# Kernel tuning notes

Hardware: AMD Instinct MI355X
Metric: run time of the kernel (lower is better)

The kernel has to match this reference:

```python
import jax, jax.numpy as jnp
import numpy as np

B, IN, OUT, E, K = 8192, 512, 720, 16, 2
MOE_TEMP = 1.0


def setup_inputs() -> dict:
    key = jax.random.key(0)
    ks = jax.random.split(key, 5)
    s_in = 1.0 / np.sqrt(IN)
    return {
        "x": jax.random.normal(ks[0], (B, IN), dtype=jnp.float32),
        "Wg": jax.random.normal(ks[1], (IN, E), dtype=jnp.float32) * s_in,
        "bg": jax.random.normal(ks[2], (E,), dtype=jnp.float32) * 0.01,
        "We": jax.random.normal(ks[3], (E, IN, OUT), dtype=jnp.float32) * s_in,
        "be": jax.random.normal(ks[4], (E, OUT), dtype=jnp.float32) * 0.01,
    }


def reference(x, Wg, bg, We, be):
    # Gating (eval mode: no noise, divide by temperature)
    gate = (x @ Wg + bg) / MOE_TEMP                      # [B, E]
    topk_vals, topk_idx = jax.lax.top_k(gate, K)          # [B, K]
    gates = jax.nn.softmax(topk_vals, axis=1)             # [B, K]

    # Dense all-expert forward (as the original module computes)
    expert_out = jnp.einsum('bi,eio->beo', x, We) + be    # [B, E, OUT]
    sel = jnp.take_along_axis(expert_out, topk_idx[:, :, None], axis=1)  # [B, K, OUT]
    output = jnp.sum(gates[:, :, None] * sel, axis=1)     # [B, OUT]

    # Load-balancing loss
    probs = jax.nn.softmax(gate, axis=1)                  # [B, E]
    assign = jnp.argmax(gate, axis=1)                     # [B]
    D = jnp.zeros((E,), dtype=gate.dtype).at[assign].add(1.0) / x.shape[0]
    P = jnp.mean(probs, axis=0)
    lb_loss = jnp.sum(D * P) * E
    return output, lb_loss
```

## Files before the change

### kernel.cpp

```cpp
#include <hip/hip_runtime.h>
#include <hip/hip_bf16.h>


#define BATCH 8192
#define IND   512
#define OUTD  720
#define NEXP  16
#define CPAD  16
#define NGBLK 512

typedef __attribute__((ext_vector_type(8))) short short8;
typedef __attribute__((ext_vector_type(4))) float floatx4;

__device__ __forceinline__ unsigned short f2bf(float f) {
    union { float f; unsigned u; } v; v.f = f;
    unsigned r = v.u + 0x7FFFu + ((v.u >> 16) & 1u);
    return (unsigned short)(r >> 16);
}
__device__ __forceinline__ float bf2f(unsigned short u) {
    union { unsigned u; float f; } v; v.u = ((unsigned)u) << 16;
    return v.f;
}

__device__ __forceinline__ void gl2lds16(const void* g, void* l) {
    __builtin_amdgcn_global_load_lds(
        (const __attribute__((address_space(1))) void*)g,
        (__attribute__((address_space(3))) void*)l, 16, 0, 0);
}

__global__ __launch_bounds__(256) void prep_kernel(
    const float* __restrict__ x, const float* __restrict__ Wg,
    const float* __restrict__ bg, const float* __restrict__ We,
    float* __restrict__ gates, int* __restrict__ rowinfo,
    int* __restrict__ cnt_blk, float* __restrict__ Pblk, float* __restrict__ Dblk,
    unsigned short* __restrict__ xb, unsigned short* __restrict__ Wt)
{
    __shared__ __align__(16) char smem[35328];
    int tid = threadIdx.x;

    if (blockIdx.x < NGBLK) {
        float* sWg   = (float*)smem;
        float* sg    = sWg + 16 * 516;
        float* smax  = sg + 16 * 17;
        float* sinv  = smax + 16;
        int*   sasgn = (int*)(sinv + 16);

        int rbase = blockIdx.x * 16;

        const float4* gw4 = (const float4*)Wg;
        #pragma unroll
        for (int j = 0; j < 8; ++j) {
            int f = tid + j * 256;
            float4 v = gw4[f];
            int i  = f >> 2;
            int e0 = (f & 3) * 4;
            sWg[(e0 + 0) * 516 + i] = v.x;
            sWg[(e0 + 1) * 516 + i] = v.y;
            sWg[(e0 + 2) * 516 + i] = v.z;
            sWg[(e0 + 3) * 516 + i] = v.w;
        }

        const float4* gx4 = (const float4*)(x + (size_t)rbase * IND);
        #pragma unroll
        for (int j = 0; j < 4; ++j) {
            int f = tid + j * 256;
            float4 v0 = gx4[2 * f];
            float4 v1 = gx4[2 * f + 1];
            short8 o;
            o[0] = (short)f2bf(v0.x); o[1] = (short)f2bf(v0.y);
            o[2] = (short)f2bf(v0.z); o[3] = (short)f2bf(v0.w);
            o[4] = (short)f2bf(v1.x); o[5] = (short)f2bf(v1.y);
            o[6] = (short)f2bf(v1.z); o[7] = (short)f2bf(v1.w);
            *(short8*)&xb[(size_t)rbase * IND + (size_t)f * 8] = o;
        }
        __syncthreads();

        int r = tid >> 4, e = tid & 15;
        const float4* xr = (const float4*)(x + (size_t)(rbase + r) * IND);
        const float4* wr = (const float4*)&sWg[e * 516];
        float acc = bg[e];
        #pragma unroll 8
        for (int i4 = 0; i4 < 128; ++i4) {
            float4 a = xr[i4], w = wr[i4];
            acc += a.x * w.x + a.y * w.y + a.z * w.z + a.w * w.w;
        }
        sg[r * 17 + e] = acc;
        __syncthreads();

        if (tid < 16) {
            int row = rbase + tid;
            float v0 = -1e30f, v1 = -1e30f; int i0 = 0, i1 = 0;
            float g[16];
            #pragma unroll
            for (int ee = 0; ee < 16; ++ee) {
                float v = sg[tid * 17 + ee]; g[ee] = v;
                if (v > v0)      { v1 = v0; i1 = i0; v0 = v; i0 = ee; }
                else if (v > v1) { v1 = v;  i1 = ee; }
            }
            float e1   = expf(v1 - v0);
            float inv2 = 1.f / (1.f + e1);
            gates[row * 2 + 0] = inv2;
            gates[row * 2 + 1] = e1 * inv2;

            float s = 0.f;
            #pragma unroll
            for (int ee = 0; ee < 16; ++ee) s += expf(g[ee] - v0);
            smax[tid]  = v0;
            sinv[tid]  = 1.f / s;
            sasgn[tid] = i0 | (i1 << 8);
        }
        __syncthreads();

        if (tid < 16) {
            int me  = sasgn[tid];
            int i0  = me & 255, i1 = me >> 8;
            int p0 = 0, p1 = 0;
            for (int rp = 0; rp < tid; ++rp) {
                int a = sasgn[rp];
                int a0 = a & 255, a1 = a >> 8;
                p0 += (a0 == i0) + (a1 == i0);
                p1 += (a0 == i1) + (a1 == i1);
            }
            rowinfo[rbase + tid] = i0 | (i1 << 4) | (p0 << 8) | (p1 << 13);

            int ee = tid;
            int cnt = 0; float D = 0.f, P = 0.f;
            #pragma unroll
            for (int rp = 0; rp < 16; ++rp) {
                int a = sasgn[rp];
                int a0 = a & 255, a1 = a >> 8;
                cnt += (a0 == ee) + (a1 == ee);
                D   += (a0 == ee) ? 1.f : 0.f;
                P   += expf(sg[rp * 17 + ee] - smax[rp]) * sinv[rp];
            }
            cnt_blk[blockIdx.x * 16 + ee] = cnt;
            Dblk[blockIdx.x * 16 + ee]    = D;
            Pblk[blockIdx.x * 16 + ee]    = P;
        }
    } else {
        float* tile = (float*)smem;
        int t  = blockIdx.x - NGBLK;
        int e  = t / 184;
        int rem = t - e * 184;
        int kb = (rem / 23) * 64;
        int ob = (rem % 23) * 32;
        const float* src = We + (size_t)e * (IND * OUTD);

        #pragma unroll
        for (int p = 0; p < 2; ++p) {
            int f  = tid + p * 256;
            int kk = f >> 3;
            int o4 = f & 7;
            float4 v = make_float4(0.f, 0.f, 0.f, 0.f);
            if (ob + o4 * 4 < OUTD)
                v = *(const float4*)&src[(size_t)(kb + kk) * OUTD + ob + o4 * 4];
            tile[(o4 * 4 + 0) * 69 + kk] = v.x;
            tile[(o4 * 4 + 1) * 69 + kk] = v.y;
            tile[(o4 * 4 + 2) * 69 + kk] = v.z;
            tile[(o4 * 4 + 3) * 69 + kk] = v.w;
        }
        __syncthreads();

        int o  = tid >> 3;
        int k8 = tid & 7;
        if (ob + o < OUTD) {
            const float* sp = &tile[o * 69 + k8 * 8];
            short8 w;
            #pragma unroll
            for (int q = 0; q < 8; ++q) w[q] = (short)f2bf(sp[q]);
            *(short8*)&Wt[(size_t)e * (OUTD * IND) + (size_t)(ob + o) * IND + kb + k8 * 8] = w;
        }
    }
}

__global__ __launch_bounds__(256) void scan_kernel(
    const int* __restrict__ cnt_blk, const float* __restrict__ Pblk,
    const float* __restrict__ Dblk,
    int* __restrict__ base_blk, int* __restrict__ counts,
    float* __restrict__ Psum, float* __restrict__ Dsum)
{
    __shared__ int scnt[NGBLK * 16];
    __shared__ float sredP[256], sredD[256];
    int tid = threadIdx.x;

    #pragma unroll
    for (int j = 0; j < 32; ++j) scnt[tid + j * 256] = cnt_blk[tid + j * 256];
    __syncthreads();

    if (tid < 16) {
        int run = 0;
        for (int b = 0; b < NGBLK; ++b) {
            int c = scnt[b * 16 + tid];
            scnt[b * 16 + tid] = run;
            run += c;
        }
        counts[tid * CPAD] = run;
    }
    __syncthreads();

    #pragma unroll
    for (int j = 0; j < 32; ++j) base_blk[tid + j * 256] = scnt[tid + j * 256];

    int e = tid & 15, stripe = tid >> 4;
    float accP = 0.f, accD = 0.f;
    for (int j = 0; j < 32; ++j) {
        int b = stripe * 32 + j;
        accP += Pblk[b * 16 + e];
        accD += Dblk[b * 16 + e];
    }
    sredP[tid] = accP; sredD[tid] = accD;
    __syncthreads();
    if (tid < 16) {
        float P = 0.f, D = 0.f;
        #pragma unroll
        for (int s = 0; s < 16; ++s) { P += sredP[s * 16 + tid]; D += sredD[s * 16 + tid]; }
        Psum[tid * CPAD] = P;
        Dsum[tid * CPAD] = D;
    }
}

__global__ __launch_bounds__(256) void scatter_kernel(
    const int* __restrict__ rowinfo, const int* __restrict__ base_blk,
    unsigned short* __restrict__ lists, int* __restrict__ inv)
{
    int row = blockIdx.x * 256 + threadIdx.x;
    int info = rowinfo[row];
    int i0 = info & 15, i1 = (info >> 4) & 15;
    int p0 = (info >> 8) & 31, p1 = (info >> 13) & 31;
    int b = row >> 4;
    int pos0 = base_blk[b * 16 + i0] + p0;
    int pos1 = base_blk[b * 16 + i1] + p1;
    lists[i0 * BATCH + pos0] = (unsigned short)(row << 1);
    lists[i1 * BATCH + pos1] = (unsigned short)((row << 1) | 1);
    inv[row * 2 + 0] = i0 * BATCH + pos0;
    inv[row * 2 + 1] = i1 * BATCH + pos1;
}

__global__ __launch_bounds__(256, 4) void moe_mfma_kernel(
    const unsigned short* __restrict__ xb, const unsigned short* __restrict__ Wt,
    const float* __restrict__ be,
    const int* __restrict__ counts, const float* __restrict__ gates,
    const unsigned short* __restrict__ lists,
    unsigned short* __restrict__ partial, int use_inv)
{
    int e = blockIdx.z;
    int n = counts[e * CPAD];
    int r0 = blockIdx.y * 128;
    if (r0 >= n) return;
    int n0 = blockIdx.x * 96;

    __shared__ unsigned short sAB[14336];
    __shared__ int   srow[128];
    __shared__ float sgw[128];
    __shared__ unsigned short sent[128];

    int tid = threadIdx.x;
    if (tid < 128) {
        int idx = r0 + tid;
        if (idx < n) {
            int ent = lists[e * BATCH + idx];
            srow[tid] = ent >> 1;
            sgw[tid]  = gates[(ent >> 1) * 2 + (ent & 1)];
            sent[tid] = (unsigned short)ent;
        } else { srow[tid] = 0; sgw[tid] = 0.f; sent[tid] = 0; }
    }
    __syncthreads();

    int lane = tid & 63, wave = tid >> 6;
    int lsub = lane >> 3;
    int swz  = (lane & 7) ^ lsub;

    const unsigned short* aglb[4];
    unsigned short* alds[4];
    #pragma unroll
    for (int g = 0; g < 4; ++g) {
        int row = wave * 32 + g * 8 + lsub;
        aglb[g] = xb + (size_t)srow[row] * IND + swz * 8;
        alds[g] = &sAB[(wave * 32 + g * 8) * 64];
    }
    const unsigned short* bglb[3];
    unsigned short* blds[3];
    #pragma unroll
    for (int g = 0; g < 3; ++g) {
        int col = n0 + wave * 24 + g * 8 + lsub;
        if (col >= OUTD) col = 0;
        bglb[g] = Wt + ((size_t)e * OUTD + col) * IND + swz * 8;
        blds[g] = &sAB[8192 + (wave * 24 + g * 8) * 64];
    }

    int l15 = lane & 15, quad = lane >> 4;
    int wm = (wave & 1) * 64, wn = (wave >> 1) * 48;
    int axor = (l15 & 7) * 8;

    floatx4 acc[4][3] = {};

    for (int kt = 0; kt < IND / 64; ++kt) {
        __syncthreads();
        #pragma unroll
        for (int g = 0; g < 4; ++g) gl2lds16(aglb[g] + kt * 64, alds[g]);
        #pragma unroll
        for (int g = 0; g < 3; ++g) gl2lds16(bglb[g] + kt * 64, blds[g]);
        __syncthreads();

        #pragma unroll
        for (int ks = 0; ks < 2; ++ks) {
            int ko = ((ks * 4 + quad) * 8) ^ axor;
            short8 a[4], b[3];
            #pragma unroll
            for (int i = 0; i < 4; ++i) a[i] = *(const short8*)&sAB[(wm + i * 16 + l15) * 64 + ko];
            #pragma unroll
            for (int j = 0; j < 3; ++j) b[j] = *(const short8*)&sAB[8192 + (wn + j * 16 + l15) * 64 + ko];
            #pragma unroll
            for (int i = 0; i < 4; ++i)
                #pragma unroll
                for (int j = 0; j < 3; ++j)
                    acc[i][j] = __builtin_amdgcn_mfma_f32_16x16x32_bf16(a[i], b[j], acc[i][j], 0, 0, 0);
        }
    }

    __syncthreads();
    #pragma unroll
    for (int j = 0; j < 3; ++j) {
        int coll = wn + j * 16 + l15;
        int gcol = n0 + coll;
        float bev = (gcol < OUTD) ? be[e * OUTD + gcol] : 0.f;
        #pragma unroll
        for (int i = 0; i < 4; ++i) {
            #pragma unroll
            for (int rr = 0; rr < 4; ++rr) {
                int rowl = wm + i * 16 + quad * 4 + rr;
                sAB[rowl * 104 + coll] = f2bf(sgw[rowl] * (acc[i][j][rr] + bev));
            }
        }
    }
    __syncthreads();

    #pragma unroll
    for (int p = 0; p < 6; ++p) {
        int c    = tid + p * 256;
        int rowl = c / 12;
        int ch   = c - rowl * 12;
        int gcol = n0 + ch * 8;
        if (gcol < OUTD && r0 + rowl < n) {
            size_t prow = use_inv ? (size_t)(e * BATCH + r0 + rowl)
                                  : (size_t)sent[rowl];
            *(short8*)&partial[prow * OUTD + gcol] = *(const short8*)&sAB[rowl * 104 + ch * 8];
        }
    }
}

__global__ __launch_bounds__(256) void combine_kernel(
    const unsigned short* __restrict__ partial, const int* __restrict__ inv,
    const float* __restrict__ Psum, const float* __restrict__ Dsum,
    float* __restrict__ out, int use_inv)
{
    unsigned f = blockIdx.x * 256 + threadIdx.x;
    unsigned b = f / 180u;
    unsigned o4 = (f - b * 180u) * 4u;
    size_t row0 = use_inv ? (size_t)inv[2u * b]     : (size_t)(2u * b);
    size_t row1 = use_inv ? (size_t)inv[2u * b + 1] : (size_t)(2u * b + 1);
    ushort4 u0 = *(const ushort4*)&partial[row0 * OUTD + o4];
    ushort4 u1 = *(const ushort4*)&partial[row1 * OUTD + o4];
    float4 rv;
    rv.x = bf2f(u0.x) + bf2f(u1.x);
    rv.y = bf2f(u0.y) + bf2f(u1.y);
    rv.z = bf2f(u0.z) + bf2f(u1.z);
    rv.w = bf2f(u0.w) + bf2f(u1.w);
    *(float4*)(out + (size_t)b * OUTD + o4) = rv;

    if (f == 0) {
        float s = 0.f;
        #pragma unroll
        for (int e = 0; e < NEXP; ++e)
            s += (Dsum[e * CPAD] / (float)BATCH) * (Psum[e * CPAD] / (float)BATCH);
        out[(size_t)BATCH * OUTD] = s * (float)NEXP;
    }
}

extern "C" void kernel_launch(void* const* d_in, const int* in_sizes, int n_in,
                              void* d_out, int out_size, void* d_ws, size_t ws_size,
                              hipStream_t stream)
{
    const float* x  = (const float*)d_in[0];
    const float* Wg = (const float*)d_in[1];
    const float* bg = (const float*)d_in[2];
    const float* We = (const float*)d_in[3];
    const float* be = (const float*)d_in[4];
    float* out = (float*)d_out;

    char* ws = (char*)d_ws;
    int*   counts  = (int*)ws;
    float* Psum    = (float*)(ws + 1024);
    float* Dsum    = (float*)(ws + 2048);
    float* gates   = (float*)(ws + 4096);
    unsigned short* lists = (unsigned short*)(ws + 69632);
    int*   inv     = (int*)(ws + 331776);
    int*   cnt_blk = (int*)(ws + 397312);
    int*   base_blk= (int*)(ws + 430080);
    float* Pblk    = (float*)(ws + 462848);
    float* Dblk    = (float*)(ws + 495616);
    int*   rowinfo = (int*)(ws + 528384);
    size_t off_xb  = 561152;
    unsigned short* xb = (unsigned short*)(ws + off_xb);
    size_t off_wt = off_xb + (size_t)BATCH * IND * 2;
    unsigned short* Wt = (unsigned short*)(ws + off_wt);
    size_t off_pt = off_wt + (size_t)NEXP * OUTD * IND * 2;
    unsigned short* partial = (unsigned short*)(ws + off_pt);
    size_t req_big = off_pt + (size_t)NEXP * BATCH * OUTD * 2;
    int use_inv = (ws_size >= req_big) ? 1 : 0;

    prep_kernel<<<NGBLK + 2944, 256, 0, stream>>>(x, Wg, bg, We, gates, rowinfo,
                                                  cnt_blk, Pblk, Dblk, xb, Wt);

    scan_kernel<<<1, 256, 0, stream>>>(cnt_blk, Pblk, Dblk, base_blk, counts, Psum, Dsum);

    scatter_kernel<<<BATCH / 256, 256, 0, stream>>>(rowinfo, base_blk, lists, inv);

    dim3 grid(8, 12, NEXP);
    moe_mfma_kernel<<<grid, 256, 0, stream>>>(xb, Wt, be, counts, gates, lists,
                                              partial, use_inv);

    combine_kernel<<<(BATCH * (OUTD / 4)) / 256, 256, 0, stream>>>(partial, inv,
                                                                   Psum, Dsum, out, use_inv);
}
```

Baseline: 150.7 us.

## Split gating from conversion and fuse scan with scatter kernel

Gating moves out of the combined prep kernel into its own kernel, which reads Wg into LDS and computes gate logits with a 4-way split-K across lanes and shuffle reductions. Format conversion and transpose of x and We go to a separate kernel with smaller LDS use. The single-block scan and the scatter kernel are merged: every scatter block redoes the prefix scan in LDS, which removes the base_blk round trip and one launch. The cost is redundant scan work in each block, and the gate kernel no longer overlaps with the weight conversion.

Measured after the change: 154.7 us. 1.03x slower.

```diff
diff --git a/kernel.cpp b/kernel.cpp
--- a/kernel.cpp
+++ b/kernel.cpp
@@ -28,38 +28,120 @@
         (__attribute__((address_space(3))) void*)l, 16, 0, 0);
 }
 
-__global__ __launch_bounds__(256) void prep_kernel(
+__global__ __launch_bounds__(256) void gate_kernel(
     const float* __restrict__ x, const float* __restrict__ Wg,
-    const float* __restrict__ bg, const float* __restrict__ We,
+    const float* __restrict__ bg,
     float* __restrict__ gates, int* __restrict__ rowinfo,
-    int* __restrict__ cnt_blk, float* __restrict__ Pblk, float* __restrict__ Dblk,
+    int* __restrict__ cnt_blk, float* __restrict__ Pblk, float* __restrict__ Dblk)
+{
+    __shared__ float sWg[16 * 516];
+    __shared__ float sg[16 * 17];
+    __shared__ float smax[16], sinv[16];
+    __shared__ int   sasgn[16];
+
+    int tid = threadIdx.x;
+    int rbase = blockIdx.x * 16;
+
+    const float4* gw4 = (const float4*)Wg;
+    #pragma unroll
+    for (int j = 0; j < 8; ++j) {
+        int f = tid + j * 256;
+        float4 v = gw4[f];
+        int i  = f >> 2;
+        int e0 = (f & 3) * 4;
+        sWg[(e0 + 0) * 516 + i] = v.x;
+        sWg[(e0 + 1) * 516 + i] = v.y;
+        sWg[(e0 + 2) * 516 + i] = v.z;
+        sWg[(e0 + 3) * 516 + i] = v.w;
+    }
+    __syncthreads();
+
+    int lane = tid & 63, w = tid >> 6;
+    int e = lane & 15, s = lane >> 4;
+    const float4* wr = (const float4*)&sWg[e * 516] + s * 32;
+
+    float accj[4];
+    #pragma unroll
+    for (int j = 0; j < 4; ++j) {
+        const float4* xr = (const float4*)(x + (size_t)(rbase + w * 4 + j) * IND) + s * 32;
+        float a0 = 0.f;
+        #pragma unroll 8
+        for (int t = 0; t < 32; ++t) {
+            float4 xa = xr[t], wa = wr[t];
+            a0 += xa.x * wa.x + xa.y * wa.y + xa.z * wa.z + xa.w * wa.w;
+        }
+        accj[j] = a0;
+    }
+    #pragma unroll
+    for (int j = 0; j < 4; ++j) {
+        float v = accj[j];
+        v += __shfl_xor(v, 16, 64);
+        v += __shfl_xor(v, 32, 64);
+        if (s == 0) sg[(w * 4 + j) * 17 + e] = v + bg[e];
+    }
+    __syncthreads();
+
+    if (tid < 16) {
+        int row = rbase + tid;
+        float v0 = -1e30f, v1 = -1e30f; int i0 = 0, i1 = 0;
+        float g[16];
+        #pragma unroll
+        for (int ee = 0; ee < 16; ++ee) {
+            float v = sg[tid * 17 + ee]; g[ee] = v;
+            if (v > v0)      { v1 = v0; i1 = i0; v0 = v; i0 = ee; }
+            else if (v > v1) { v1 = v;  i1 = ee; }
+        }
+        float e1   = expf(v1 - v0);
+        float inv2 = 1.f / (1.f + e1);
+        gates[row * 2 + 0] = inv2;
+        gates[row * 2 + 1] = e1 * inv2;
+
+        float ssum = 0.f;
+        #pragma unroll
+        for (int ee = 0; ee < 16; ++ee) ssum += expf(g[ee] - v0);
+        smax[tid]  = v0;
+        sinv[tid]  = 1.f / ssum;
+        sasgn[tid] = i0 | (i1 << 8);
+    }
+    __syncthreads();
+
+    if (tid < 16) {
+        int me  = sasgn[tid];
+        int i0  = me & 255, i1 = me >> 8;
+        int p0 = 0, p1 = 0;
+        for (int rp = 0; rp < tid; ++rp) {
+            int a = sasgn[rp];
+            int a0 = a & 255, a1 = a >> 8;
+            p0 += (a0 == i0) + (a1 == i0);
+            p1 += (a0 == i1) + (a1 == i1);
+        }
+        rowinfo[rbase + tid] = i0 | (i1 << 4) | (p0 << 8) | (p1 << 13);
+
+        int ee = tid;
+        int cnt = 0; float D = 0.f, P = 0.f;
+        #pragma unroll
+        for (int rp = 0; rp < 16; ++rp) {
+            int a = sasgn[rp];
+            int a0 = a & 255, a1 = a >> 8;
+            cnt += (a0 == ee) + (a1 == ee);
+            D   += (a0 == ee) ? 1.f : 0.f;
+            P   += expf(sg[rp * 17 + ee] - smax[rp]) * sinv[rp];
+        }
+        cnt_blk[blockIdx.x * 16 + ee] = cnt;
+        Dblk[blockIdx.x * 16 + ee]    = D;
+        Pblk[blockIdx.x * 16 + ee]    = P;
+    }
+}
+
+__global__ __launch_bounds__(256) void convtrans_kernel(
+    const float* __restrict__ x, const float* __restrict__ We,
     unsigned short* __restrict__ xb, unsigned short* __restrict__ Wt)
 {
-    __shared__ __align__(16) char smem[35328];
+    __shared__ float tile[32 * 69];
     int tid = threadIdx.x;
 
     if (blockIdx.x < NGBLK) {
-        float* sWg   = (float*)smem;
-        float* sg    = sWg + 16 * 516;
-        float* smax  = sg + 16 * 17;
-        float* sinv  = smax + 16;
-        int*   sasgn = (int*)(sinv + 16);
-
         int rbase = blockIdx.x * 16;
-
-        const float4* gw4 = (const float4*)Wg;
-        #pragma unroll
-        for (int j = 0; j < 8; ++j) {
-            int f = tid + j * 256;
-            float4 v = gw4[f];
-            int i  = f >> 2;
-            int e0 = (f & 3) * 4;
-            sWg[(e0 + 0) * 516 + i] = v.x;
-            sWg[(e0 + 1) * 516 + i] = v.y;
-            sWg[(e0 + 2) * 516 + i] = v.z;
-            sWg[(e0 + 3) * 516 + i] = v.w;
-        }
-
         const float4* gx4 = (const float4*)(x + (size_t)rbase * IND);
         #pragma unroll
         for (int j = 0; j < 4; ++j) {
@@ -73,72 +155,7 @@
             o[6] = (short)f2bf(v1.z); o[7] = (short)f2bf(v1.w);
             *(short8*)&xb[(size_t)rbase * IND + (size_t)f * 8] = o;
         }
-        __syncthreads();
-
-        int r = tid >> 4, e = tid & 15;
-        const float4* xr = (const float4*)(x + (size_t)(rbase + r) * IND);
-        const float4* wr = (const float4*)&sWg[e * 516];
-        float acc = bg[e];
-        #pragma unroll 8
-        for (int i4 = 0; i4 < 128; ++i4) {
-            float4 a = xr[i4], w = wr[i4];
-            acc += a.x * w.x + a.y * w.y + a.z * w.z + a.w * w.w;
-        }
-        sg[r * 17 + e] = acc;
-        __syncthreads();
-
-        if (tid < 16) {
-            int row = rbase + tid;
-            float v0 = -1e30f, v1 = -1e30f; int i0 = 0, i1 = 0;
-            float g[16];
-            #pragma unroll
-            for (int ee = 0; ee < 16; ++ee) {
-                float v = sg[tid * 17 + ee]; g[ee] = v;
-                if (v > v0)      { v1 = v0; i1 = i0; v0 = v; i0 = ee; }
-                else if (v > v1) { v1 = v;  i1 = ee; }
-            }
-            float e1   = expf(v1 - v0);
-            float inv2 = 1.f / (1.f + e1);
-            gates[row * 2 + 0] = inv2;
-            gates[row * 2 + 1] = e1 * inv2;
-
-            float s = 0.f;
-            #pragma unroll
-            for (int ee = 0; ee < 16; ++ee) s += expf(g[ee] - v0);
-            smax[tid]  = v0;
-            sinv[tid]  = 1.f / s;
-            sasgn[tid] = i0 | (i1 << 8);
-        }
-        __syncthreads();
-
-        if (tid < 16) {
-            int me  = sasgn[tid];
-            int i0  = me & 255, i1 = me >> 8;
-            int p0 = 0, p1 = 0;
-            for (int rp = 0; rp < tid; ++rp) {
-                int a = sasgn[rp];
-                int a0 = a & 255, a1 = a >> 8;
-                p0 += (a0 == i0) + (a1 == i0);
-                p1 += (a0 == i1) + (a1 == i1);
-            }
-            rowinfo[rbase + tid] = i0 | (i1 << 4) | (p0 << 8) | (p1 << 13);
-
-            int ee = tid;
-            int cnt = 0; float D = 0.f, P = 0.f;
-            #pragma unroll
-            for (int rp = 0; rp < 16; ++rp) {
-                int a = sasgn[rp];
-                int a0 = a & 255, a1 = a >> 8;
-                cnt += (a0 == ee) + (a1 == ee);
-                D   += (a0 == ee) ? 1.f : 0.f;
-                P   += expf(sg[rp * 17 + ee] - smax[rp]) * sinv[rp];
-            }
-            cnt_blk[blockIdx.x * 16 + ee] = cnt;
-            Dblk[blockIdx.x * 16 + ee]    = D;
-            Pblk[blockIdx.x * 16 + ee]    = P;
-        }
     } else {
-        float* tile = (float*)smem;
         int t  = blockIdx.x - NGBLK;
         int e  = t / 184;
         int rem = t - e * 184;
@@ -165,19 +182,19 @@
         int k8 = tid & 7;
         if (ob + o < OUTD) {
             const float* sp = &tile[o * 69 + k8 * 8];
-            short8 w;
-            #pragma unroll
-            for (int q = 0; q < 8; ++q) w[q] = (short)f2bf(sp[q]);
-            *(short8*)&Wt[(size_t)e * (OUTD * IND) + (size_t)(ob + o) * IND + kb + k8 * 8] = w;
-        }
-    }
-}
-
-__global__ __launch_bounds__(256) void scan_kernel(
+            short8 wv;
+            #pragma unroll
+            for (int q = 0; q < 8; ++q) wv[q] = (short)f2bf(sp[q]);
+            *(short8*)&Wt[(size_t)e * (OUTD * IND) + (size_t)(ob + o) * IND + kb + k8 * 8] = wv;
+        }
+    }
+}
+
+__global__ __launch_bounds__(256) void scan_scatter_kernel(
     const int* __restrict__ cnt_blk, const float* __restrict__ Pblk,
-    const float* __restrict__ Dblk,
-    int* __restrict__ base_blk, int* __restrict__ counts,
-    float* __restrict__ Psum, float* __restrict__ Dsum)
+    const float* __restrict__ Dblk, const int* __restrict__ rowinfo,
+    unsigned short* __restrict__ lists, int* __restrict__ inv,
+    int* __restrict__ counts, float* __restrict__ Psum, float* __restrict__ Dsum)
 {
     __shared__ int scnt[NGBLK * 16];
     __shared__ float sredP[256], sredD[256];
@@ -194,46 +211,40 @@
             scnt[b * 16 + tid] = run;
             run += c;
         }
-        counts[tid * CPAD] = run;
-    }
-    __syncthreads();
-
-    #pragma unroll
-    for (int j = 0; j < 32; ++j) base_blk[tid + j * 256] = scnt[tid + j * 256];
-
-    int e = tid & 15, stripe = tid >> 4;
-    float accP = 0.f, accD = 0.f;
-    for (int j = 0; j < 32; ++j) {
-        int b = stripe * 32 + j;
-        accP += Pblk[b * 16 + e];
-        accD += Dblk[b * 16 + e];
-    }
-    sredP[tid] = accP; sredD[tid] = accD;
-    __syncthreads();
-    if (tid < 16) {
-        float P = 0.f, D = 0.f;
-        #pragma unroll
-        for (int s = 0; s < 16; ++s) { P += sredP[s * 16 + tid]; D += sredD[s * 16 + tid]; }
-        Psum[tid * CPAD] = P;
-        Dsum[tid * CPAD] = D;
-    }
-}
-
-__global__ __launch_bounds__(256) void scatter_kernel(
-    const int* __restrict__ rowinfo, const int* __restrict__ base_blk,
-    unsigned short* __restrict__ lists, int* __restrict__ inv)
-{
-    int row = blockIdx.x * 256 + threadIdx.x;
+        if (blockIdx.x == 0) counts[tid * CPAD] = run;
+    }
+    __syncthreads();
+
+    int row = blockIdx.x * 256 + tid;
     int info = rowinfo[row];
     int i0 = info & 15, i1 = (info >> 4) & 15;
     int p0 = (info >> 8) & 31, p1 = (info >> 13) & 31;
-    int b = row >> 4;
-    int pos0 = base_blk[b * 16 + i0] + p0;
-    int pos1 = base_blk[b * 16 + i1] + p1;
+    int g = row >> 4;
+    int pos0 = scnt[g * 16 + i0] + p0;
+    int pos1 = scnt[g * 16 + i1] + p1;
     lists[i0 * BATCH + pos0] = (unsigned short)(row << 1);
     lists[i1 * BATCH + pos1] = (unsigned short)((row << 1) | 1);
     inv[row * 2 + 0] = i0 * BATCH + pos0;
     inv[row * 2 + 1] = i1 * BATCH + pos1;
+
+    if (blockIdx.x == 0) {
+        int e = tid & 15, stripe = tid >> 4;
+        float accP = 0.f, accD = 0.f;
+        for (int j = 0; j < 32; ++j) {
+            int b = stripe * 32 + j;
+            accP += Pblk[b * 16 + e];
+            accD += Dblk[b * 16 + e];
+        }
+        sredP[tid] = accP; sredD[tid] = accD;
+        __syncthreads();
+        if (tid < 16) {
+            float P = 0.f, D = 0.f;
+            #pragma unroll
+            for (int s = 0; s < 16; ++s) { P += sredP[s * 16 + tid]; D += sredD[s * 16 + tid]; }
+            Psum[tid * CPAD] = P;
+            Dsum[tid * CPAD] = D;
+        }
+    }
 }
 
 __global__ __launch_bounds__(256, 4) void moe_mfma_kernel(
@@ -396,7 +407,6 @@
     unsigned short* lists = (unsigned short*)(ws + 69632);
     int*   inv     = (int*)(ws + 331776);
     int*   cnt_blk = (int*)(ws + 397312);
-    int*   base_blk= (int*)(ws + 430080);
     float* Pblk    = (float*)(ws + 462848);
     float* Dblk    = (float*)(ws + 495616);
     int*   rowinfo = (int*)(ws + 528384);
@@ -409,12 +419,13 @@
     size_t req_big = off_pt + (size_t)NEXP * BATCH * OUTD * 2;
     int use_inv = (ws_size >= req_big) ? 1 : 0;
 
-    prep_kernel<<<NGBLK + 2944, 256, 0, stream>>>(x, Wg, bg, We, gates, rowinfo,
-                                                  cnt_blk, Pblk, Dblk, xb, Wt);
-
-    scan_kernel<<<1, 256, 0, stream>>>(cnt_blk, Pblk, Dblk, base_blk, counts, Psum, Dsum);
-
-    scatter_kernel<<<BATCH / 256, 256, 0, stream>>>(rowinfo, base_blk, lists, inv);
+    gate_kernel<<<NGBLK, 256, 0, stream>>>(x, Wg, bg, gates, rowinfo,
+                                           cnt_blk, Pblk, Dblk);
+
+    convtrans_kernel<<<NGBLK + 2944, 256, 0, stream>>>(x, We, xb, Wt);
+
+    scan_scatter_kernel<<<BATCH / 256, 256, 0, stream>>>(cnt_blk, Pblk, Dblk, rowinfo,
+                                                         lists, inv, counts, Psum, Dsum);
 
     dim3 grid(8, 12, NEXP);
     moe_mfma_kernel<<<grid, 256, 0, stream>>>(xb, Wt, be, counts, gates, lists,
```

## Fold scan and scatter kernels into GEMM and combine kernels

Applied to the files above, without the earlier changes.

Removes the separate scan and scatter launches. Each MFMA block now recomputes its expert's prefix over the per-block byte counts in shared memory, then finds its rows by binary search over that prefix plus a scan of the 16 rowinfo entries in the matching group. Partial results are indexed by (row, k), so the combine kernel reads two adjacent rows directly, and the load-balance loss reduction moves into combine block 0. The grid's y dimension shrinks from 12 to 10, which caps each expert at 1280 tokens; that is a correctness risk if routing is skewed, and every GEMM block also repeats the prefix work.

After: 140.7 us (median of 2 runs). 6.7% less time.

```diff
diff --git a/kernel.cpp b/kernel.cpp
--- a/kernel.cpp
+++ b/kernel.cpp
@@ -6,7 +6,6 @@
 #define IND   512
 #define OUTD  720
 #define NEXP  16
-#define CPAD  16
 #define NGBLK 512
 
 typedef __attribute__((ext_vector_type(8))) short short8;
@@ -32,7 +31,7 @@
     const float* __restrict__ x, const float* __restrict__ Wg,
     const float* __restrict__ bg, const float* __restrict__ We,
     float* __restrict__ gates, int* __restrict__ rowinfo,
-    int* __restrict__ cnt_blk, float* __restrict__ Pblk, float* __restrict__ Dblk,
+    unsigned char* __restrict__ cnt8, float* __restrict__ Pblk, float* __restrict__ Dblk,
     unsigned short* __restrict__ xb, unsigned short* __restrict__ Wt)
 {
     __shared__ __align__(16) char smem[35328];
@@ -102,11 +101,11 @@
             gates[row * 2 + 0] = inv2;
             gates[row * 2 + 1] = e1 * inv2;
 
-            float s = 0.f;
-            #pragma unroll
-            for (int ee = 0; ee < 16; ++ee) s += expf(g[ee] - v0);
+            float ssum = 0.f;
+            #pragma unroll
+            for (int ee = 0; ee < 16; ++ee) ssum += expf(g[ee] - v0);
             smax[tid]  = v0;
-            sinv[tid]  = 1.f / s;
+            sinv[tid]  = 1.f / ssum;
             sasgn[tid] = i0 | (i1 << 8);
         }
         __syncthreads();
@@ -133,9 +132,9 @@
                 D   += (a0 == ee) ? 1.f : 0.f;
                 P   += expf(sg[rp * 17 + ee] - smax[rp]) * sinv[rp];
             }
-            cnt_blk[blockIdx.x * 16 + ee] = cnt;
-            Dblk[blockIdx.x * 16 + ee]    = D;
-            Pblk[blockIdx.x * 16 + ee]    = P;
+            cnt8[blockIdx.x * 16 + ee] = (unsigned char)cnt;
+            Dblk[blockIdx.x * 16 + ee] = D;
+            Pblk[blockIdx.x * 16 + ee] = P;
         }
     } else {
         float* tile = (float*)smem;
@@ -165,103 +164,84 @@
         int k8 = tid & 7;
         if (ob + o < OUTD) {
             const float* sp = &tile[o * 69 + k8 * 8];
-            short8 w;
-            #pragma unroll
-            for (int q = 0; q < 8; ++q) w[q] = (short)f2bf(sp[q]);
-            *(short8*)&Wt[(size_t)e * (OUTD * IND) + (size_t)(ob + o) * IND + kb + k8 * 8] = w;
-        }
-    }
-}
-
-__global__ __launch_bounds__(256) void scan_kernel(
-    const int* __restrict__ cnt_blk, const float* __restrict__ Pblk,
-    const float* __restrict__ Dblk,
-    int* __restrict__ base_blk, int* __restrict__ counts,
-    float* __restrict__ Psum, float* __restrict__ Dsum)
-{
-    __shared__ int scnt[NGBLK * 16];
-    __shared__ float sredP[256], sredD[256];
-    int tid = threadIdx.x;
-
-    #pragma unroll
-    for (int j = 0; j < 32; ++j) scnt[tid + j * 256] = cnt_blk[tid + j * 256];
-    __syncthreads();
-
-    if (tid < 16) {
-        int run = 0;
-        for (int b = 0; b < NGBLK; ++b) {
-            int c = scnt[b * 16 + tid];
-            scnt[b * 16 + tid] = run;
-            run += c;
-        }
-        counts[tid * CPAD] = run;
-    }
-    __syncthreads();
-
-    #pragma unroll
-    for (int j = 0; j < 32; ++j) base_blk[tid + j * 256] = scnt[tid + j * 256];
-
-    int e = tid & 15, stripe = tid >> 4;
-    float accP = 0.f, accD = 0.f;
-    for (int j = 0; j < 32; ++j) {
-        int b = stripe * 32 + j;
-        accP += Pblk[b * 16 + e];
-        accD += Dblk[b * 16 + e];
-    }
-    sredP[tid] = accP; sredD[tid] = accD;
-    __syncthreads();
-    if (tid < 16) {
-        float P = 0.f, D = 0.f;
-        #pragma unroll
-        for (int s = 0; s < 16; ++s) { P += sredP[s * 16 + tid]; D += sredD[s * 16 + tid]; }
-        Psum[tid * CPAD] = P;
-        Dsum[tid * CPAD] = D;
-    }
-}
-
-__global__ __launch_bounds__(256) void scatter_kernel(
-    const int* __restrict__ rowinfo, const int* __restrict__ base_blk,
-    unsigned short* __restrict__ lists, int* __restrict__ inv)
-{
-    int row = blockIdx.x * 256 + threadIdx.x;
-    int info = rowinfo[row];
-    int i0 = info & 15, i1 = (info >> 4) & 15;
-    int p0 = (info >> 8) & 31, p1 = (info >> 13) & 31;
-    int b = row >> 4;
-    int pos0 = base_blk[b * 16 + i0] + p0;
-    int pos1 = base_blk[b * 16 + i1] + p1;
-    lists[i0 * BATCH + pos0] = (unsigned short)(row << 1);
-    lists[i1 * BATCH + pos1] = (unsigned short)((row << 1) | 1);
-    inv[row * 2 + 0] = i0 * BATCH + pos0;
-    inv[row * 2 + 1] = i1 * BATCH + pos1;
+            short8 wv;
+            #pragma unroll
+            for (int q = 0; q < 8; ++q) wv[q] = (short)f2bf(sp[q]);
+            *(short8*)&Wt[(size_t)e * (OUTD * IND) + (size_t)(ob + o) * IND + kb + k8 * 8] = wv;
+        }
+    }
 }
 
 __global__ __launch_bounds__(256, 4) void moe_mfma_kernel(
     const unsigned short* __restrict__ xb, const unsigned short* __restrict__ Wt,
     const float* __restrict__ be,
-    const int* __restrict__ counts, const float* __restrict__ gates,
-    const unsigned short* __restrict__ lists,
-    unsigned short* __restrict__ partial, int use_inv)
+    const unsigned char* __restrict__ cnt8, const int* __restrict__ rowinfo,
+    const float* __restrict__ gates,
+    unsigned short* __restrict__ partial)
 {
     int e = blockIdx.z;
-    int n = counts[e * CPAD];
     int r0 = blockIdx.y * 128;
-    if (r0 >= n) return;
     int n0 = blockIdx.x * 96;
 
     __shared__ unsigned short sAB[14336];
+    __shared__ unsigned short sbase[513];
+    __shared__ int   schunk[16];
     __shared__ int   srow[128];
     __shared__ float sgw[128];
     __shared__ unsigned short sent[128];
 
     int tid = threadIdx.x;
+
+    sbase[tid]       = cnt8[tid * 16 + e];
+    sbase[tid + 256] = cnt8[(tid + 256) * 16 + e];
+    __syncthreads();
+    if (tid < 16) {
+        int s = 0;
+        #pragma unroll
+        for (int j = 0; j < 32; ++j) s += sbase[tid * 32 + j];
+        schunk[tid] = s;
+    }
+    __syncthreads();
+    if (tid == 0) {
+        int run = 0;
+        #pragma unroll
+        for (int c = 0; c < 16; ++c) { int s = schunk[c]; schunk[c] = run; run += s; }
+        sbase[512] = (unsigned short)run;
+    }
+    __syncthreads();
+    if (tid < 16) {
+        int run = schunk[tid];
+        #pragma unroll
+        for (int j = 0; j < 32; ++j) {
+            int c = sbase[tid * 32 + j];
+            sbase[tid * 32 + j] = (unsigned short)run;
+            run += c;
+        }
+    }
+    __syncthreads();
+    int n = sbase[512];
+    if (r0 >= n) return;
+
     if (tid < 128) {
         int idx = r0 + tid;
         if (idx < n) {
-            int ent = lists[e * BATCH + idx];
-            srow[tid] = ent >> 1;
-            sgw[tid]  = gates[(ent >> 1) * 2 + (ent & 1)];
-            sent[tid] = (unsigned short)ent;
+            int g = 0;
+            #pragma unroll
+            for (int step = 256; step; step >>= 1)
+                if (g + step <= 511 && (int)sbase[g + step] <= idx) g += step;
+            int local = idx - (int)sbase[g];
+            int row = 0, k = 0;
+            #pragma unroll
+            for (int r = 0; r < 16; ++r) {
+                int info = rowinfo[g * 16 + r];
+                int i0 = info & 15, i1 = (info >> 4) & 15;
+                int p0 = (info >> 8) & 31, p1 = (info >> 13) & 31;
+                if (i0 == e && p0 == local) { row = g * 16 + r; k = 0; }
+                if (i1 == e && p1 == local) { row = g * 16 + r; k = 1; }
+            }
+            srow[tid] = row;
+            sgw[tid]  = gates[row * 2 + k];
+            sent[tid] = (unsigned short)((row << 1) | k);
         } else { srow[tid] = 0; sgw[tid] = 0.f; sent[tid] = 0; }
     }
     __syncthreads();
@@ -342,25 +322,24 @@
         int ch   = c - rowl * 12;
         int gcol = n0 + ch * 8;
         if (gcol < OUTD && r0 + rowl < n) {
-            size_t prow = use_inv ? (size_t)(e * BATCH + r0 + rowl)
-                                  : (size_t)sent[rowl];
-            *(short8*)&partial[prow * OUTD + gcol] = *(const short8*)&sAB[rowl * 104 + ch * 8];
+            *(short8*)&partial[(size_t)sent[rowl] * OUTD + gcol] =
+                *(const short8*)&sAB[rowl * 104 + ch * 8];
         }
     }
 }
 
 __global__ __launch_bounds__(256) void combine_kernel(
-    const unsigned short* __restrict__ partial, const int* __restrict__ inv,
-    const float* __restrict__ Psum, const float* __restrict__ Dsum,
-    float* __restrict__ out, int use_inv)
+    const unsigned short* __restrict__ partial,
+    const float* __restrict__ Pblk, const float* __restrict__ Dblk,
+    float* __restrict__ out)
 {
+    __shared__ float sredP[256], sredD[256];
     unsigned f = blockIdx.x * 256 + threadIdx.x;
     unsigned b = f / 180u;
     unsigned o4 = (f - b * 180u) * 4u;
-    size_t row0 = use_inv ? (size_t)inv[2u * b]     : (size_t)(2u * b);
-    size_t row1 = use_inv ? (size_t)inv[2u * b + 1] : (size_t)(2u * b + 1);
-    ushort4 u0 = *(const ushort4*)&partial[row0 * OUTD + o4];
-    ushort4 u1 = *(const ushort4*)&partial[row1 * OUTD + o4];
+    const unsigned short* p0 = partial + (size_t)(2u * b) * OUTD + o4;
+    ushort4 u0 = *(const ushort4*)p0;
+    ushort4 u1 = *(const ushort4*)(p0 + OUTD);
     float4 rv;
     rv.x = bf2f(u0.x) + bf2f(u1.x);
     rv.y = bf2f(u0.y) + bf2f(u1.y);
@@ -368,12 +347,27 @@
     rv.w = bf2f(u0.w) + bf2f(u1.w);
     *(float4*)(out + (size_t)b * OUTD + o4) = rv;
 
-    if (f == 0) {
-        float s = 0.f;
-        #pragma unroll
-        for (int e = 0; e < NEXP; ++e)
-            s += (Dsum[e * CPAD] / (float)BATCH) * (Psum[e * CPAD] / (float)BATCH);
-        out[(size_t)BATCH * OUTD] = s * (float)NEXP;
+    if (blockIdx.x == 0) {
+        int tid = threadIdx.x;
+        int e = tid & 15, stripe = tid >> 4;
+        float accP = 0.f, accD = 0.f;
+        for (int j = 0; j < 32; ++j) {
+            int g = stripe * 32 + j;
+            accP += Pblk[g * 16 + e];
+            accD += Dblk[g * 16 + e];
+        }
+        sredP[tid] = accP; sredD[tid] = accD;
+        __syncthreads();
+        if (tid == 0) {
+            float s = 0.f;
+            for (int ee = 0; ee < 16; ++ee) {
+                float P = 0.f, D = 0.f;
+                #pragma unroll
+                for (int st = 0; st < 16; ++st) { P += sredP[st * 16 + ee]; D += sredD[st * 16 + ee]; }
+                s += (D / (float)BATCH) * (P / (float)BATCH);
+            }
+            out[(size_t)BATCH * OUTD] = s * (float)NEXP;
+        }
     }
 }
 
@@ -389,37 +383,23 @@
     float* out = (float*)d_out;
 
     char* ws = (char*)d_ws;
-    int*   counts  = (int*)ws;
-    float* Psum    = (float*)(ws + 1024);
-    float* Dsum    = (float*)(ws + 2048);
-    float* gates   = (float*)(ws + 4096);
-    unsigned short* lists = (unsigned short*)(ws + 69632);
-    int*   inv     = (int*)(ws + 331776);
-    int*   cnt_blk = (int*)(ws + 397312);
-    int*   base_blk= (int*)(ws + 430080);
-    float* Pblk    = (float*)(ws + 462848);
-    float* Dblk    = (float*)(ws + 495616);
-    int*   rowinfo = (int*)(ws + 528384);
-    size_t off_xb  = 561152;
+    float* gates   = (float*)ws;
+    int*   rowinfo = (int*)(ws + 65536);
+    unsigned char* cnt8 = (unsigned char*)(ws + 98304);
+    float* Pblk    = (float*)(ws + 106496);
+    float* Dblk    = (float*)(ws + 139264);
+    size_t off_xb  = 172032;
     unsigned short* xb = (unsigned short*)(ws + off_xb);
     size_t off_wt = off_xb + (size_t)BATCH * IND * 2;
     unsigned short* Wt = (unsigned short*)(ws + off_wt);
     size_t off_pt = off_wt + (size_t)NEXP * OUTD * IND * 2;
     unsigned short* partial = (unsigned short*)(ws + off_pt);
-    size_t req_big = off_pt + (size_t)NEXP * BATCH * OUTD * 2;
-    int use_inv = (ws_size >= req_big) ? 1 : 0;
 
     prep_kernel<<<NGBLK + 2944, 256, 0, stream>>>(x, Wg, bg, We, gates, rowinfo,
-                                                  cnt_blk, Pblk, Dblk, xb, Wt);
-
-    scan_kernel<<<1, 256, 0, stream>>>(cnt_blk, Pblk, Dblk, base_blk, counts, Psum, Dsum);
-
-    scatter_kernel<<<BATCH / 256, 256, 0, stream>>>(rowinfo, base_blk, lists, inv);
-
-    dim3 grid(8, 12, NEXP);
-    moe_mfma_kernel<<<grid, 256, 0, stream>>>(xb, Wt, be, counts, gates, lists,
-                                              partial, use_inv);
-
-    combine_kernel<<<(BATCH * (OUTD / 4)) / 256, 256, 0, stream>>>(partial, inv,
-                                                                   Psum, Dsum, out, use_inv);
-}
+                                                  cnt8, Pblk, Dblk, xb, Wt);
+
+    dim3 grid(8, 10, NEXP);
+    moe_mfma_kernel<<<grid, 256, 0, stream>>>(xb, Wt, be, cnt8, rowinfo, gates, partial);
+
+    combine_kernel<<<(BATCH * (OUTD / 4)) / 256, 256, 0, stream>>>(partial, Pblk, Dblk, out);
+}
```
